# Optimization experiments

Hardware: AMD Instinct MI355X
Metric: run time of the kernel (lower is better)

## Reference

```python
import jax, jax.numpy as jnp
import numpy as np

N_NODE = 50000
N_EDGE = 800000
D = 64       # in_dim = out_dim = hidden_dim
A = 64       # attn_dim
N_REL = 475  # 2*237+1 relation ids
B = 32       # batch of queries


def setup_inputs() -> dict:
    key = jax.random.key(0)
    ks = jax.random.split(key, 16)
    hidden = jax.random.normal(ks[0], (N_NODE, D), dtype=jnp.float32)
    sub = jax.random.randint(ks[1], (N_EDGE,), 0, N_NODE)
    rel = jax.random.randint(ks[2], (N_EDGE,), 0, N_REL)
    obj = jax.random.randint(ks[3], (N_EDGE,), 0, N_NODE)
    edges = jnp.stack([sub, rel, obj], axis=1)  # [E, 3]
    gnn_emb_rel = jax.random.normal(ks[4], (N_REL, D), dtype=jnp.float32)
    mapping = jax.random.randint(ks[5], (N_REL,), 0, N_REL)  # rel id -> unique-rel row
    q_rel = jax.random.randint(ks[6], (B,), 0, N_REL)
    r_idx = jax.random.randint(ks[7], (N_EDGE,), 0, B)  # edge -> query index
    s = 1.0 / np.sqrt(D)
    sa = 1.0 / np.sqrt(A)
    u = lambda k, shape, b: jax.random.uniform(k, shape, jnp.float32, minval=-b, maxval=b)
    return {
        "hidden": hidden,
        "edges": edges,
        "gnn_emb_rel": gnn_emb_rel,
        "mapping": mapping,
        "q_rel": q_rel,
        "r_idx": r_idx,
        "n_node": N_NODE,
        "Ws_w": u(ks[8], (A, D), s),
        "Wr_w": u(ks[9], (A, D), s),
        "Wqr_w": u(ks[10], (A, D), s),
        "Wqr_b": u(ks[11], (A,), s),
        "walpha_w": u(ks[12], (1, A), sa),
        "walpha_b": u(ks[13], (1,), sa),
        "Wh_w": u(ks[14], (D, D), s),
    }


def reference(hidden, edges, gnn_emb_rel, mapping, q_rel, r_idx, n_node,
              Ws_w, Wr_w, Wqr_w, Wqr_b, walpha_w, walpha_b, Wh_w):
    sub, rel, obj = edges[:, 0], edges[:, 1], edges[:, 2]
    hs = hidden[sub]                       # [E, D] gather
    hr = gnn_emb_rel[mapping[rel]]         # [E, D] gather
    # per-query h_qr projected once, then gathered per edge (same math, cheaper)
    hq = gnn_emb_rel[mapping[q_rel]]       # [B, D]
    qr_attn = hq @ Wqr_w.T + Wqr_b         # [B, A]
    pre = hs @ Ws_w.T + hr @ Wr_w.T + qr_attn[r_idx]   # [E, A]
    alpha = jax.nn.sigmoid(jax.nn.relu(pre) @ walpha_w.T + walpha_b)  # [E, 1]
    message = alpha * (hs * hr)            # [E, D]
    message_agg = jax.ops.segment_sum(message, obj, num_segments=n_node)  # [N, D]
    hidden_new = jax.nn.relu(message_agg @ Wh_w.T)  # act = ReLU from GNN_auto
    return hidden_new
```

## Files before the change

kernel.cpp:

```cpp
#include <hip/hip_runtime.h>
#include <hip/hip_bf16.h>

#define D64 64
#define WTP 65
#define LPAD 68

typedef __attribute__((ext_vector_type(8))) short short8;
typedef __attribute__((ext_vector_type(4))) float f32x4;

__device__ inline float lane_bcast(float v, int l) {
    return __uint_as_float(__builtin_amdgcn_readlane(__float_as_uint(v), l));
}
__device__ inline float bf16_lo(unsigned u) { return __uint_as_float(u << 16); }
__device__ inline float bf16_hi(unsigned u) { return __uint_as_float(u & 0xFFFF0000u); }
__device__ inline float bf16u(unsigned short u) { return __uint_as_float((unsigned)u << 16); }
__device__ inline unsigned short f2bf(float f) {
    __hip_bfloat16 b = __float2bfloat16(f);
    return *(unsigned short*)&b;
}

__global__ void prep_kernel(const float* __restrict__ emb, const int* __restrict__ mapping,
                            const int* __restrict__ q_rel,
                            const float* __restrict__ Wr, const float* __restrict__ Wqr,
                            const float* __restrict__ Wqr_b, const float* __restrict__ Ws,
                            unsigned short* __restrict__ hrmapb,
                            unsigned short* __restrict__ hrWb,
                            unsigned short* __restrict__ qrb,
                            unsigned short* __restrict__ WsB,
                            int* __restrict__ counts, int nrel, int nq, int NN) {
    int b = blockIdx.x;
    int lane = threadIdx.x;
    if (b < nrel) {
        int m = mapping[b];
        float v = emb[m * D64 + lane];
        hrmapb[b * D64 + lane] = f2bf(v);
        float acc = 0.f;
#pragma unroll
        for (int d = 0; d < D64; ++d)
            acc = fmaf(lane_bcast(v, d), Wr[lane * D64 + d], acc);
        hrWb[b * D64 + lane] = f2bf(acc);
    } else if (b < nrel + nq) {
        int q = b - nrel;
        int m = mapping[q_rel[q]];
        float v = emb[m * D64 + lane];
        float acc = Wqr_b[lane];
#pragma unroll
        for (int d = 0; d < D64; ++d)
            acc = fmaf(lane_bcast(v, d), Wqr[lane * D64 + d], acc);
        qrb[q * D64 + lane] = f2bf(acc);
    } else if (b < nrel + nq + 64) {
        int c = b - nrel - nq;
        WsB[c * D64 + lane] = f2bf(Ws[c * D64 + lane]);
    } else {
        int c = b - nrel - nq - 64;
        int idx = c * 64 + lane;
        if (idx < NN) counts[idx] = 0;
    }
}

__global__ void comb_kernel(const unsigned short* __restrict__ hrWb,
                            const unsigned short* __restrict__ qrb,
                            unsigned short* __restrict__ combb, int nrel) {
    int i = blockIdx.x * blockDim.x + threadIdx.x;
    int total = nrel * 32 * D64;
    if (i < total) {
        int lane = i & 63;
        int row = i >> 6;
        int r = row >> 5;
        int q = row & 31;
        combb[i] = f2bf(bf16u(hrWb[r * D64 + lane]) + bf16u(qrb[q * D64 + lane]));
    }
}

__global__ void rowmm_mfma_kernel(const float* __restrict__ in,
                                  const unsigned short* __restrict__ WsB,
                                  unsigned short* __restrict__ outb,
                                  unsigned short* __restrict__ inb, int nrows) {
    __shared__ unsigned short la[16 * LPAD];
    int lane = threadIdx.x;
    int rbase = blockIdx.x * 16;
    if (rbase >= nrows) return;

    short8 bfrag[8];
#pragma unroll
    for (int t = 0; t < 4; ++t)
#pragma unroll
        for (int kk = 0; kk < 2; ++kk)
            bfrag[t * 2 + kk] = *(const short8*)(WsB + (size_t)(t * 16 + (lane & 15)) * D64 +
                                                 kk * 32 + (lane >> 4) * 8);

#pragma unroll
    for (int rr = 0; rr < 16; ++rr) {
        int r = rbase + rr;
        float v = (r < nrows) ? in[(size_t)r * D64 + lane] : 0.f;
        unsigned short bb = f2bf(v);
        if (r < nrows) inb[(size_t)r * D64 + lane] = bb;
        la[rr * LPAD + lane] = bb;
    }

    f32x4 acc[4];
#pragma unroll
    for (int t = 0; t < 4; ++t) acc[t] = (f32x4){0.f, 0.f, 0.f, 0.f};
#pragma unroll
    for (int kk = 0; kk < 2; ++kk) {
        short8 afrag = *(const short8*)(la + (lane & 15) * LPAD + kk * 32 + (lane >> 4) * 8);
#pragma unroll
        for (int t = 0; t < 4; ++t)
            acc[t] = __builtin_amdgcn_mfma_f32_16x16x32_bf16(afrag, bfrag[t * 2 + kk],
                                                             acc[t], 0, 0, 0);
    }
#pragma unroll
    for (int t = 0; t < 4; ++t)
#pragma unroll
        for (int reg = 0; reg < 4; ++reg) {
            int row = rbase + (lane >> 4) * 4 + reg;
            int col = t * 16 + (lane & 15);
            if (row < nrows)
                outb[(size_t)row * D64 + col] = f2bf(acc[t][reg]);
        }
}

__global__ void hist_pack_kernel(const int* __restrict__ edges, const int* __restrict__ r_idx,
                                 int* __restrict__ counts, uint2* __restrict__ epack, int E) {
    int i4 = blockIdx.x * blockDim.x + threadIdx.x;
    int n4 = E >> 2;
    if (i4 < n4) {
        const uint4* e4 = (const uint4*)edges;
        uint4 a = e4[i4 * 3 + 0];
        uint4 b = e4[i4 * 3 + 1];
        uint4 c = e4[i4 * 3 + 2];
        uint4 r = ((const uint4*)r_idx)[i4];
        uint4 p01 = make_uint4(a.x | ((((a.y << 5) | r.x)) << 17), a.z,
                               a.w | ((((b.x << 5) | r.y)) << 17), b.y);
        uint4 p23 = make_uint4(b.z | ((((b.w << 5) | r.z)) << 17), c.x,
                               c.y | ((((c.z << 5) | r.w)) << 17), c.w);
        ((uint4*)epack)[i4 * 2 + 0] = p01;
        ((uint4*)epack)[i4 * 2 + 1] = p23;
        atomicAdd(&counts[a.z], 1);
        atomicAdd(&counts[b.y], 1);
        atomicAdd(&counts[c.x], 1);
        atomicAdd(&counts[c.w], 1);
    }
    int tail = n4 * 4;
    int ti = tail + i4;
    if (i4 < (E - tail) && ti < E) {
        unsigned sub = edges[ti * 3 + 0];
        unsigned rel = edges[ti * 3 + 1];
        unsigned obj = edges[ti * 3 + 2];
        unsigned ri  = r_idx[ti];
        epack[ti] = make_uint2(sub | (((rel << 5) | ri) << 17), obj);
        atomicAdd(&counts[obj], 1);
    }
}

__global__ void scan1_kernel(const int* __restrict__ counts, int* __restrict__ offs,
                             int* __restrict__ partials, int n) {
    __shared__ int tsum[256];
    int t = threadIdx.x;
    int base = blockIdx.x * 1024 + t * 4;
    int v[4];
    int s = 0;
#pragma unroll
    for (int i = 0; i < 4; ++i) {
        int idx = base + i;
        int c = (idx < n) ? counts[idx] : 0;
        v[i] = s;
        s += c;
    }
    tsum[t] = s;
    __syncthreads();
    for (int off = 1; off < 256; off <<= 1) {
        int y = (t >= off) ? tsum[t - off] : 0;
        __syncthreads();
        tsum[t] += y;
        __syncthreads();
    }
    int incl = tsum[t];
    int thread_prefix = incl - s;
    if (t == 255) partials[blockIdx.x] = incl;
#pragma unroll
    for (int i = 0; i < 4; ++i) {
        int idx = base + i;
        if (idx < n) offs[idx] = thread_prefix + v[i];
    }
}

__global__ void scan2_kernel(int* partials, int nb) {
    int t = threadIdx.x;
    int own = (t < nb) ? partials[t] : 0;
    int v = own;
    for (int off = 1; off < 64; off <<= 1) {
        int y = __shfl_up(v, off, 64);
        if (t >= off) v += y;
    }
    if (t < nb) partials[t] = v - own;
}

__global__ void scan3_kernel(int* __restrict__ offs, const int* __restrict__ partials, int n) {
    int base = blockIdx.x * 1024 + threadIdx.x;
    int add = partials[blockIdx.x];
#pragma unroll
    for (int i = 0; i < 4; ++i) {
        int idx = base + i * 256;
        if (idx < n) offs[idx] += add;
    }
}

__global__ void alpha_scatter_kernel(const uint2* __restrict__ epack,
                                     const unsigned short* __restrict__ hsWb,
                                     const unsigned short* __restrict__ combb,
                                     const float* __restrict__ walpha_w,
                                     const float* __restrict__ walpha_b,
                                     int* __restrict__ offs, int2* __restrict__ rec,
                                     int E, int half) {
    int tid = blockIdx.x * blockDim.x + threadIdx.x;
    int e0 = tid >> 3;
    int l = tid & 7;
    if (e0 >= half) return;
    int e1 = e0 + half;
    bool has1 = (e1 < E);

    uint2 p0 = epack[e0];
    uint2 p1 = has1 ? epack[e1] : make_uint2(0u, 0u);
    unsigned sub0 = p0.x & 0x1FFFF, comb0 = p0.x >> 17;
    unsigned sub1 = p1.x & 0x1FFFF, comb1 = p1.x >> 17;
    int obj0 = (int)p0.y, obj1 = (int)p1.y;

    uint4 hv0 = *(const uint4*)(hsWb  + (size_t)sub0  * D64 + l * 8);
    uint4 cv0 = *(const uint4*)(combb + (size_t)comb0 * D64 + l * 8);
    uint4 hv1 = *(const uint4*)(hsWb  + (size_t)sub1  * D64 + l * 8);
    uint4 cv1 = *(const uint4*)(combb + (size_t)comb1 * D64 + l * 8);
    const float4* w = (const float4*)(walpha_w + l * 8);
    float4 w0 = w[0], w1 = w[1];

    float x0, x1;
    x0 = fmaxf(bf16_lo(hv0.x) + bf16_lo(cv0.x), 0.f) * w0.x;
    x0 = fmaf(fmaxf(bf16_hi(hv0.x) + bf16_hi(cv0.x), 0.f), w0.y, x0);
    x0 = fmaf(fmaxf(bf16_lo(hv0.y) + bf16_lo(cv0.y), 0.f), w0.z, x0);
    x0 = fmaf(fmaxf(bf16_hi(hv0.y) + bf16_hi(cv0.y), 0.f), w0.w, x0);
    x0 = fmaf(fmaxf(bf16_lo(hv0.z) + bf16_lo(cv0.z), 0.f), w1.x, x0);
    x0 = fmaf(fmaxf(bf16_hi(hv0.z) + bf16_hi(cv0.z), 0.f), w1.y, x0);
    x0 = fmaf(fmaxf(bf16_lo(hv0.w) + bf16_lo(cv0.w), 0.f), w1.z, x0);
    x0 = fmaf(fmaxf(bf16_hi(hv0.w) + bf16_hi(cv0.w), 0.f), w1.w, x0);

    x1 = fmaxf(bf16_lo(hv1.x) + bf16_lo(cv1.x), 0.f) * w0.x;
    x1 = fmaf(fmaxf(bf16_hi(hv1.x) + bf16_hi(cv1.x), 0.f), w0.y, x1);
    x1 = fmaf(fmaxf(bf16_lo(hv1.y) + bf16_lo(cv1.y), 0.f), w0.z, x1);
    x1 = fmaf(fmaxf(bf16_hi(hv1.y) + bf16_hi(cv1.y), 0.f), w0.w, x1);
    x1 = fmaf(fmaxf(bf16_lo(hv1.z) + bf16_lo(cv1.z), 0.f), w1.x, x1);
    x1 = fmaf(fmaxf(bf16_hi(hv1.z) + bf16_hi(cv1.z), 0.f), w1.y, x1);
    x1 = fmaf(fmaxf(bf16_lo(hv1.w) + bf16_lo(cv1.w), 0.f), w1.z, x1);
    x1 = fmaf(fmaxf(bf16_hi(hv1.w) + bf16_hi(cv1.w), 0.f), w1.w, x1);

    x0 += __shfl_xor(x0, 4, 64);
    x1 += __shfl_xor(x1, 4, 64);
    x0 += __shfl_xor(x0, 2, 64);
    x1 += __shfl_xor(x1, 2, 64);
    x0 += __shfl_xor(x0, 1, 64);
    x1 += __shfl_xor(x1, 1, 64);

    if (l == 0) {
        float wb = walpha_b[0];
        float a0 = 1.f / (1.f + __expf(-(x0 + wb)));
        int rel0 = comb0 >> 5;
        int slot0 = atomicAdd(&offs[obj0], 1);
        rec[slot0] = make_int2((int)(sub0 | (rel0 << 17)), __float_as_int(a0));
        if (has1) {
            float a1 = 1.f / (1.f + __expf(-(x1 + wb)));
            int rel1 = comb1 >> 5;
            int slot1 = atomicAdd(&offs[obj1], 1);
            rec[slot1] = make_int2((int)(sub1 | (rel1 << 17)), __float_as_int(a1));
        }
    }
}

__global__ void agg_wh_kernel(const int2* __restrict__ rec, const int* __restrict__ endoff,
                              const unsigned short* __restrict__ hiddenb,
                              const unsigned short* __restrict__ hrmapb,
                              const float* __restrict__ Wh,
                              float* __restrict__ out, int NN) {
    __shared__ float WT[D64 * WTP];
    int tid = threadIdx.x;
    for (int i = tid; i < D64 * D64; i += blockDim.x)
        WT[(i & 63) * WTP + (i >> 6)] = Wh[i];
    __syncthreads();
    int lane = tid & 63;
    int n = (blockIdx.x * blockDim.x + tid) >> 6;
    if (n >= NN) return;
    int start = (n == 0) ? 0 : endoff[n - 1];
    int end = endoff[n];
    start = __builtin_amdgcn_readfirstlane(start);
    end = __builtin_amdgcn_readfirstlane(end);
    float acc0 = 0.f, acc1 = 0.f, acc2 = 0.f, acc3 = 0.f;
    for (int base = start; base < end; base += 64) {
        int cnt = end - base;
        if (cnt > 64) cnt = 64;
        int rx = 0, ry = 0;
        if (lane < cnt) {
            int2 r = rec[base + lane];
            rx = r.x; ry = r.y;
        }
        int j = 0;
        for (; j + 7 < cnt; j += 8) {
            int a_rx[8], a_ry[8];
#pragma unroll
            for (int k = 0; k < 8; ++k) {
                a_rx[k] = __builtin_amdgcn_readlane(rx, j + k);
                a_ry[k] = __builtin_amdgcn_readlane(ry, j + k);
            }
            float h[8], m[8];
#pragma unroll
            for (int k = 0; k < 8; ++k) {
                h[k] = bf16u(hiddenb[(size_t)(a_rx[k] & 0x1FFFF) * D64 + lane]);
                m[k] = bf16u(hrmapb[(size_t)((unsigned)a_rx[k] >> 17) * D64 + lane]);
            }
            acc0 = fmaf(__uint_as_float(a_ry[0]) * h[0], m[0], acc0);
            acc1 = fmaf(__uint_as_float(a_ry[1]) * h[1], m[1], acc1);
            acc2 = fmaf(__uint_as_float(a_ry[2]) * h[2], m[2], acc2);
            acc3 = fmaf(__uint_as_float(a_ry[3]) * h[3], m[3], acc3);
            acc0 = fmaf(__uint_as_float(a_ry[4]) * h[4], m[4], acc0);
            acc1 = fmaf(__uint_as_float(a_ry[5]) * h[5], m[5], acc1);
            acc2 = fmaf(__uint_as_float(a_ry[6]) * h[6], m[6], acc2);
            acc3 = fmaf(__uint_as_float(a_ry[7]) * h[7], m[7], acc3);
        }
        for (; j + 3 < cnt; j += 4) {
            int rx0 = __builtin_amdgcn_readlane(rx, j);
            int ry0 = __builtin_amdgcn_readlane(ry, j);
            int rx1 = __builtin_amdgcn_readlane(rx, j + 1);
            int ry1 = __builtin_amdgcn_readlane(ry, j + 1);
            int rx2 = __builtin_amdgcn_readlane(rx, j + 2);
            int ry2 = __builtin_amdgcn_readlane(ry, j + 2);
            int rx3 = __builtin_amdgcn_readlane(rx, j + 3);
            int ry3 = __builtin_amdgcn_readlane(ry, j + 3);
            float h0 = bf16u(hiddenb[(size_t)(rx0 & 0x1FFFF) * D64 + lane]);
            float m0 = bf16u(hrmapb[(size_t)((unsigned)rx0 >> 17) * D64 + lane]);
            float h1 = bf16u(hiddenb[(size_t)(rx1 & 0x1FFFF) * D64 + lane]);
            float m1 = bf16u(hrmapb[(size_t)((unsigned)rx1 >> 17) * D64 + lane]);
            float h2 = bf16u(hiddenb[(size_t)(rx2 & 0x1FFFF) * D64 + lane]);
            float m2 = bf16u(hrmapb[(size_t)((unsigned)rx2 >> 17) * D64 + lane]);
            float h3 = bf16u(hiddenb[(size_t)(rx3 & 0x1FFFF) * D64 + lane]);
            float m3 = bf16u(hrmapb[(size_t)((unsigned)rx3 >> 17) * D64 + lane]);
            acc0 = fmaf(__uint_as_float(ry0) * h0, m0, acc0);
            acc1 = fmaf(__uint_as_float(ry1) * h1, m1, acc1);
            acc2 = fmaf(__uint_as_float(ry2) * h2, m2, acc2);
            acc3 = fmaf(__uint_as_float(ry3) * h3, m3, acc3);
        }
        for (; j < cnt; ++j) {
            int rx0 = __builtin_amdgcn_readlane(rx, j);
            int ry0 = __builtin_amdgcn_readlane(ry, j);
            float h0 = bf16u(hiddenb[(size_t)(rx0 & 0x1FFFF) * D64 + lane]);
            float m0 = bf16u(hrmapb[(size_t)((unsigned)rx0 >> 17) * D64 + lane]);
            acc0 = fmaf(__uint_as_float(ry0) * h0, m0, acc0);
        }
    }
    float acc = (acc0 + acc1) + (acc2 + acc3);
    float o = 0.f;
#pragma unroll
    for (int d = 0; d < D64; ++d)
        o = fmaf(lane_bcast(acc, d), WT[d * WTP + lane], o);
    out[(size_t)n * D64 + lane] = fmaxf(o, 0.f);
}

extern "C" void kernel_launch(void* const* d_in, const int* in_sizes, int n_in,
                              void* d_out, int out_size, void* d_ws, size_t ws_size,
                              hipStream_t stream) {
    const float* hidden   = (const float*)d_in[0];
    const int*   edges    = (const int*)d_in[1];
    const float* emb_rel  = (const float*)d_in[2];
    const int*   mapping  = (const int*)d_in[3];
    const int*   q_rel    = (const int*)d_in[4];
    const int*   r_idx    = (const int*)d_in[5];
    const float* Ws_w     = (const float*)d_in[7];
    const float* Wr_w     = (const float*)d_in[8];
    const float* Wqr_w    = (const float*)d_in[9];
    const float* Wqr_b    = (const float*)d_in[10];
    const float* walpha_w = (const float*)d_in[11];
    const float* walpha_b = (const float*)d_in[12];
    const float* Wh_w     = (const float*)d_in[13];
    float* out = (float*)d_out;

    int NN   = in_sizes[0] / D64;
    int E    = in_sizes[5];
    int NREL = in_sizes[3];
    int NQ   = in_sizes[4];

    char* ws = (char*)d_ws;
    size_t off = 0;
    unsigned short* hsWb    = (unsigned short*)(ws + off); off += (size_t)NN * D64 * 2;
    unsigned short* hiddenb = (unsigned short*)(ws + off); off += (size_t)NN * D64 * 2;
    int2*  rec  = (int2*)(ws + off);       off += (size_t)E * sizeof(int2);
    uint2* epack = (uint2*)(ws + off);     off += (size_t)E * sizeof(uint2);
    int* counts = (int*)(ws + off);        off += (size_t)NN * sizeof(int);
    int* offs   = (int*)(ws + off);        off += (size_t)NN * sizeof(int);
    int* partials = (int*)(ws + off);      off += 64 * sizeof(int);
    unsigned short* hrmapb = (unsigned short*)(ws + off); off += (size_t)NREL * D64 * 2;
    unsigned short* hrWb   = (unsigned short*)(ws + off); off += (size_t)NREL * D64 * 2;
    unsigned short* qrb    = (unsigned short*)(ws + off); off += (size_t)NQ * D64 * 2;
    unsigned short* WsB    = (unsigned short*)(ws + off); off += (size_t)D64 * D64 * 2;
    unsigned short* combb  = (unsigned short*)(ws + off); off += (size_t)NREL * 32 * D64 * 2;

    int NB = (NN + 1023) / 1024;

    {
        int zblocks = (NN + 63) / 64;
        prep_kernel<<<NREL + NQ + 64 + zblocks, 64, 0, stream>>>(
            emb_rel, mapping, q_rel, Wr_w, Wqr_w, Wqr_b, Ws_w,
            hrmapb, hrWb, qrb, WsB, counts, NREL, NQ, NN);
    }
    comb_kernel<<<(NREL * 32 * D64 + 255) / 256, 256, 0, stream>>>(hrWb, qrb, combb, NREL);
    rowmm_mfma_kernel<<<(NN + 15) / 16, 64, 0, stream>>>(hidden, WsB, hsWb, hiddenb, NN);
    {
        int n4 = (E + 3) / 4;
        hist_pack_kernel<<<(n4 + 255) / 256, 256, 0, stream>>>(edges, r_idx, counts, epack, E);
    }
    scan1_kernel<<<NB, 256, 0, stream>>>(counts, offs, partials, NN);
    scan2_kernel<<<1, 64, 0, stream>>>(partials, NB);
    scan3_kernel<<<NB, 256, 0, stream>>>(offs, partials, NN);
    {
        int half = (E + 1) / 2;
        long long threads = (long long)half * 8;
        int blocks = (int)((threads + 255) / 256);
        alpha_scatter_kernel<<<blocks, 256, 0, stream>>>(epack, hsWb, combb,
                                                         walpha_w, walpha_b, offs, rec, E, half);
    }
    agg_wh_kernel<<<(NN * 64 + 1023) / 1024, 1024, 0, stream>>>(rec, offs, hiddenb, hrmapb,
                                                                Wh_w, out, NN);
}
```

Baseline: 156.7 us.

## Split Wh projection into MFMA kernel and fuse edge packing into rowmm

The aggregation kernel no longer does a per-lane 64-step FMA projection with an LDS-staged transposed Wh. It now writes the bf16 aggregate into reused workspace (the epack region), and a new MFMA bf16 kernel applies Wh and ReLU. Separately, the hist/pack pass is folded into the hidden-projection MFMA kernel through a grid-stride loop, which removes one launch. The costs are an extra launch plus an NN×64 bf16 round trip through memory, and bf16 rounding of the aggregate before the projection.

```diff
diff --git a/kernel.cpp b/kernel.cpp
--- a/kernel.cpp
+++ b/kernel.cpp
@@ -2,7 +2,6 @@
 #include <hip/hip_bf16.h>
 
 #define D64 64
-#define WTP 65
 #define LPAD 68
 
 typedef __attribute__((ext_vector_type(8))) short short8;
@@ -23,10 +22,12 @@
                             const int* __restrict__ q_rel,
                             const float* __restrict__ Wr, const float* __restrict__ Wqr,
                             const float* __restrict__ Wqr_b, const float* __restrict__ Ws,
+                            const float* __restrict__ Wh,
                             unsigned short* __restrict__ hrmapb,
                             unsigned short* __restrict__ hrWb,
                             unsigned short* __restrict__ qrb,
                             unsigned short* __restrict__ WsB,
+                            unsigned short* __restrict__ WhB,
                             int* __restrict__ counts, int nrel, int nq, int NN) {
     int b = blockIdx.x;
     int lane = threadIdx.x;
@@ -51,8 +52,11 @@
     } else if (b < nrel + nq + 64) {
         int c = b - nrel - nq;
         WsB[c * D64 + lane] = f2bf(Ws[c * D64 + lane]);
+    } else if (b < nrel + nq + 128) {
+        int c = b - nrel - nq - 64;
+        WhB[c * D64 + lane] = f2bf(Wh[c * D64 + lane]);
     } else {
-        int c = b - nrel - nq - 64;
+        int c = b - nrel - nq - 128;
         int idx = c * 64 + lane;
         if (idx < NN) counts[idx] = 0;
     }
@@ -75,57 +79,56 @@
 __global__ void rowmm_mfma_kernel(const float* __restrict__ in,
                                   const unsigned short* __restrict__ WsB,
                                   unsigned short* __restrict__ outb,
-                                  unsigned short* __restrict__ inb, int nrows) {
+                                  unsigned short* __restrict__ inb, int nrows,
+                                  const int* __restrict__ edges, const int* __restrict__ r_idx,
+                                  int* __restrict__ counts, uint2* __restrict__ epack, int E) {
     __shared__ unsigned short la[16 * LPAD];
     int lane = threadIdx.x;
     int rbase = blockIdx.x * 16;
-    if (rbase >= nrows) return;
-
-    short8 bfrag[8];
-#pragma unroll
-    for (int t = 0; t < 4; ++t)
-#pragma unroll
-        for (int kk = 0; kk < 2; ++kk)
-            bfrag[t * 2 + kk] = *(const short8*)(WsB + (size_t)(t * 16 + (lane & 15)) * D64 +
-                                                 kk * 32 + (lane >> 4) * 8);
-
-#pragma unroll
-    for (int rr = 0; rr < 16; ++rr) {
-        int r = rbase + rr;
-        float v = (r < nrows) ? in[(size_t)r * D64 + lane] : 0.f;
-        unsigned short bb = f2bf(v);
-        if (r < nrows) inb[(size_t)r * D64 + lane] = bb;
-        la[rr * LPAD + lane] = bb;
-    }
-
-    f32x4 acc[4];
-#pragma unroll
-    for (int t = 0; t < 4; ++t) acc[t] = (f32x4){0.f, 0.f, 0.f, 0.f};
-#pragma unroll
-    for (int kk = 0; kk < 2; ++kk) {
-        short8 afrag = *(const short8*)(la + (lane & 15) * LPAD + kk * 32 + (lane >> 4) * 8);
+
+    if (rbase < nrows) {
+        short8 bfrag[8];
 #pragma unroll
         for (int t = 0; t < 4; ++t)
-            acc[t] = __builtin_amdgcn_mfma_f32_16x16x32_bf16(afrag, bfrag[t * 2 + kk],
-                                                             acc[t], 0, 0, 0);
-    }
-#pragma unroll
-    for (int t = 0; t < 4; ++t)
-#pragma unroll
-        for (int reg = 0; reg < 4; ++reg) {
-            int row = rbase + (lane >> 4) * 4 + reg;
-            int col = t * 16 + (lane & 15);
-            if (row < nrows)
-                outb[(size_t)row * D64 + col] = f2bf(acc[t][reg]);
-        }
-}
-
-__global__ void hist_pack_kernel(const int* __restrict__ edges, const int* __restrict__ r_idx,
-                                 int* __restrict__ counts, uint2* __restrict__ epack, int E) {
-    int i4 = blockIdx.x * blockDim.x + threadIdx.x;
+#pragma unroll
+            for (int kk = 0; kk < 2; ++kk)
+                bfrag[t * 2 + kk] = *(const short8*)(WsB + (size_t)(t * 16 + (lane & 15)) * D64 +
+                                                     kk * 32 + (lane >> 4) * 8);
+
+#pragma unroll
+        for (int rr = 0; rr < 16; ++rr) {
+            int r = rbase + rr;
+            float v = (r < nrows) ? in[(size_t)r * D64 + lane] : 0.f;
+            unsigned short bb = f2bf(v);
+            if (r < nrows) inb[(size_t)r * D64 + lane] = bb;
+            la[rr * LPAD + lane] = bb;
+        }
+
+        f32x4 acc[4];
+#pragma unroll
+        for (int t = 0; t < 4; ++t) acc[t] = (f32x4){0.f, 0.f, 0.f, 0.f};
+#pragma unroll
+        for (int kk = 0; kk < 2; ++kk) {
+            short8 afrag = *(const short8*)(la + (lane & 15) * LPAD + kk * 32 + (lane >> 4) * 8);
+#pragma unroll
+            for (int t = 0; t < 4; ++t)
+                acc[t] = __builtin_amdgcn_mfma_f32_16x16x32_bf16(afrag, bfrag[t * 2 + kk],
+                                                                 acc[t], 0, 0, 0);
+        }
+#pragma unroll
+        for (int t = 0; t < 4; ++t)
+#pragma unroll
+            for (int reg = 0; reg < 4; ++reg) {
+                int row = rbase + (lane >> 4) * 4 + reg;
+                int col = t * 16 + (lane & 15);
+                if (row < nrows)
+                    outb[(size_t)row * D64 + col] = f2bf(acc[t][reg]);
+            }
+    }
+
     int n4 = E >> 2;
-    if (i4 < n4) {
-        const uint4* e4 = (const uint4*)edges;
+    const uint4* e4 = (const uint4*)edges;
+    for (int i4 = blockIdx.x * 64 + lane; i4 < n4; i4 += gridDim.x * 64) {
         uint4 a = e4[i4 * 3 + 0];
         uint4 b = e4[i4 * 3 + 1];
         uint4 c = e4[i4 * 3 + 2];
@@ -142,8 +145,9 @@
         atomicAdd(&counts[c.w], 1);
     }
     int tail = n4 * 4;
-    int ti = tail + i4;
-    if (i4 < (E - tail) && ti < E) {
+    int gt = blockIdx.x * 64 + lane;
+    int ti = tail + gt;
+    if (gt < (E - tail) && ti < E) {
         unsigned sub = edges[ti * 3 + 0];
         unsigned rel = edges[ti * 3 + 1];
         unsigned obj = edges[ti * 3 + 2];
@@ -274,16 +278,11 @@
     }
 }
 
-__global__ void agg_wh_kernel(const int2* __restrict__ rec, const int* __restrict__ endoff,
-                              const unsigned short* __restrict__ hiddenb,
-                              const unsigned short* __restrict__ hrmapb,
-                              const float* __restrict__ Wh,
-                              float* __restrict__ out, int NN) {
-    __shared__ float WT[D64 * WTP];
+__global__ void agg_kernel(const int2* __restrict__ rec, const int* __restrict__ endoff,
+                           const unsigned short* __restrict__ hiddenb,
+                           const unsigned short* __restrict__ hrmapb,
+                           unsigned short* __restrict__ aggb, int NN) {
     int tid = threadIdx.x;
-    for (int i = tid; i < D64 * D64; i += blockDim.x)
-        WT[(i & 63) * WTP + (i >> 6)] = Wh[i];
-    __syncthreads();
     int lane = tid & 63;
     int n = (blockIdx.x * blockDim.x + tid) >> 6;
     if (n >= NN) return;
@@ -353,12 +352,45 @@
             acc0 = fmaf(__uint_as_float(ry0) * h0, m0, acc0);
         }
     }
-    float acc = (acc0 + acc1) + (acc2 + acc3);
-    float o = 0.f;
-#pragma unroll
-    for (int d = 0; d < D64; ++d)
-        o = fmaf(lane_bcast(acc, d), WT[d * WTP + lane], o);
-    out[(size_t)n * D64 + lane] = fmaxf(o, 0.f);
+    aggb[(size_t)n * D64 + lane] = f2bf((acc0 + acc1) + (acc2 + acc3));
+}
+
+__global__ void rowmm_wh_kernel(const unsigned short* __restrict__ aggb,
+                                const unsigned short* __restrict__ WhB,
+                                float* __restrict__ out, int nrows) {
+    int lane = threadIdx.x;
+    int rbase = blockIdx.x * 16;
+    if (rbase >= nrows) return;
+
+    short8 bfrag[8];
+#pragma unroll
+    for (int t = 0; t < 4; ++t)
+#pragma unroll
+        for (int kk = 0; kk < 2; ++kk)
+            bfrag[t * 2 + kk] = *(const short8*)(WhB + (size_t)(t * 16 + (lane & 15)) * D64 +
+                                                 kk * 32 + (lane >> 4) * 8);
+
+    f32x4 acc[4];
+#pragma unroll
+    for (int t = 0; t < 4; ++t) acc[t] = (f32x4){0.f, 0.f, 0.f, 0.f};
+#pragma unroll
+    for (int kk = 0; kk < 2; ++kk) {
+        short8 afrag = *(const short8*)(aggb + (size_t)(rbase + (lane & 15)) * D64 +
+                                        kk * 32 + (lane >> 4) * 8);
+#pragma unroll
+        for (int t = 0; t < 4; ++t)
+            acc[t] = __builtin_amdgcn_mfma_f32_16x16x32_bf16(afrag, bfrag[t * 2 + kk],
+                                                             acc[t], 0, 0, 0);
+    }
+#pragma unroll
+    for (int t = 0; t < 4; ++t)
+#pragma unroll
+        for (int reg = 0; reg < 4; ++reg) {
+            int row = rbase + (lane >> 4) * 4 + reg;
+            int col = t * 16 + (lane & 15);
+            if (row < nrows)
+                out[(size_t)row * D64 + col] = fmaxf(acc[t][reg], 0.f);
+        }
 }
 
 extern "C" void kernel_launch(void* const* d_in, const int* in_sizes, int n_in,
@@ -390,6 +422,7 @@
     unsigned short* hiddenb = (unsigned short*)(ws + off); off += (size_t)NN * D64 * 2;
     int2*  rec  = (int2*)(ws + off);       off += (size_t)E * sizeof(int2);
     uint2* epack = (uint2*)(ws + off);     off += (size_t)E * sizeof(uint2);
+    unsigned short* aggb = (unsigned short*)epack;
     int* counts = (int*)(ws + off);        off += (size_t)NN * sizeof(int);
     int* offs   = (int*)(ws + off);        off += (size_t)NN * sizeof(int);
     int* partials = (int*)(ws + off);      off += 64 * sizeof(int);
@@ -397,22 +430,20 @@
     unsigned short* hrWb   = (unsigned short*)(ws + off); off += (size_t)NREL * D64 * 2;
     unsigned short* qrb    = (unsigned short*)(ws + off); off += (size_t)NQ * D64 * 2;
     unsigned short* WsB    = (unsigned short*)(ws + off); off += (size_t)D64 * D64 * 2;
+    unsigned short* WhB    = (unsigned short*)(ws + off); off += (size_t)D64 * D64 * 2;
     unsigned short* combb  = (unsigned short*)(ws + off); off += (size_t)NREL * 32 * D64 * 2;
 
     int NB = (NN + 1023) / 1024;
 
     {
         int zblocks = (NN + 63) / 64;
-        prep_kernel<<<NREL + NQ + 64 + zblocks, 64, 0, stream>>>(
-            emb_rel, mapping, q_rel, Wr_w, Wqr_w, Wqr_b, Ws_w,
-            hrmapb, hrWb, qrb, WsB, counts, NREL, NQ, NN);
+        prep_kernel<<<NREL + NQ + 128 + zblocks, 64, 0, stream>>>(
+            emb_rel, mapping, q_rel, Wr_w, Wqr_w, Wqr_b, Ws_w, Wh_w,
+            hrmapb, hrWb, qrb, WsB, WhB, counts, NREL, NQ, NN);
     }
     comb_kernel<<<(NREL * 32 * D64 + 255) / 256, 256, 0, stream>>>(hrWb, qrb, combb, NREL);
-    rowmm_mfma_kernel<<<(NN + 15) / 16, 64, 0, stream>>>(hidden, WsB, hsWb, hiddenb, NN);
-    {
-        int n4 = (E + 3) / 4;
-        hist_pack_kernel<<<(n4 + 255) / 256, 256, 0, stream>>>(edges, r_idx, counts, epack, E);
-    }
+    rowmm_mfma_kernel<<<(NN + 15) / 16, 64, 0, stream>>>(hidden, WsB, hsWb, hiddenb, NN,
+                                                         edges, r_idx, counts, epack, E);
     scan1_kernel<<<NB, 256, 0, stream>>>(counts, offs, partials, NN);
     scan2_kernel<<<1, 64, 0, stream>>>(partials, NB);
     scan3_kernel<<<NB, 256, 0, stream>>>(offs, partials, NN);
@@ -423,6 +454,7 @@
         alpha_scatter_kernel<<<blocks, 256, 0, stream>>>(epack, hsWb, combb,
                                                          walpha_w, walpha_b, offs, rec, E, half);
     }
-    agg_wh_kernel<<<(NN * 64 + 1023) / 1024, 1024, 0, stream>>>(rec, offs, hiddenb, hrmapb,
-                                                                Wh_w, out, NN);
-}
+    agg_kernel<<<(NN * 64 + 1023) / 1024, 1024, 0, stream>>>(rec, offs, hiddenb, hrmapb,
+                                                             aggb, NN);
+    rowmm_wh_kernel<<<(NN + 15) / 16, 64, 0, stream>>>(aggb, WhB, out, NN);
+}
```

Result: faster. 143.7 us (-8.3%).
